# Kernel optimization log

Hardware: AMD Instinct MI355X
Metric: run time of the kernel (lower is better)

The kernel has to match this reference:

```python
import jax, jax.numpy as jnp
import numpy as np

N_QUBITS = 12
N_LAYERS = 2
PATCH = 16
NPS = 14  # patches per side for 224/16
N_PATCHES = NPS * NPS
SCALE = 1.0 / np.sqrt(N_QUBITS)


def _butterfly_gates(n):
    # Faithful replication of QuantumOrthogonalLayer.butterfly_circuit indexing:
    # param_idx increments even when the (idx1, idx2) pair is skipped.
    gates, pidx = [], 0
    n_bl = int(np.ceil(np.log2(n)))
    for layer in range(n_bl):
        stride = 2 ** layer
        for start in range(0, n - stride, 2 * stride):
            for off in range(stride):
                i1, i2 = start + off, start + off + stride
                if i1 < n and i2 < n:
                    gates.append((pidx, i1, i2))
                pidx += 1
    nppl = sum(2 ** (n_bl - 1 - i) * 2 ** i for i in range(n_bl))  # n_params() = 32
    return gates, nppl

GATES, NPPL = _butterfly_gates(N_QUBITS)

# Pauli-Z sign table: qubit 0 is the most-significant bit of the flattened state index.
_bits = (np.arange(2 ** N_QUBITS)[:, None] >> np.arange(N_QUBITS - 1, -1, -1)[None, :]) & 1
Z_SIGNS = jnp.asarray(1.0 - 2.0 * _bits, dtype=jnp.float32)  # (4096, 12)


def _rbs_u(theta):
    # 4x4 real unitary of RY(2t,w1); CNOT(w1,w2); RY(-2t,w1); CNOT(w1,w2)
    c, s = jnp.cos(theta), jnp.sin(theta)
    c2, s2, cs = c * c, s * s, c * s
    return jnp.stack([
        jnp.stack([c2, s2, -cs, cs]),
        jnp.stack([s2, c2, cs, -cs]),
        jnp.stack([cs, -cs, c2, s2]),
        jnp.stack([-cs, cs, s2, c2]),
    ])


def _apply_2q(state, U, i, j):
    # state: (P, 2, 2, ..., 2); apply U to qubit axes i, j
    st = jnp.moveaxis(state, (1 + i, 1 + j), (-2, -1))
    shp = st.shape
    st = st.reshape(shp[:-2] + (4,)) @ U.T
    return jnp.moveaxis(st.reshape(shp), (-2, -1), (1 + i, 1 + j))


@jax.checkpoint
def quantum_expvals(features, params):
    # features: (P, n_qubits) angles; params: (N_LAYERS * NPPL,)
    P = features.shape[0]
    half = 0.5 * features
    amp = jnp.stack([jnp.cos(half), jnp.sin(half)], axis=-1)  # (P, n, 2) RY(x)|0>
    state = jnp.ones((P, 1), features.dtype)
    for q in range(N_QUBITS):  # product-state angle encoding
        state = (state[:, :, None] * amp[:, q][:, None, :]).reshape(P, -1)
    state = state.reshape((P,) + (2,) * N_QUBITS)
    for l in range(N_LAYERS):
        base = l * NPPL
        for pidx, w1, w2 in GATES:
            state = _apply_2q(state, _rbs_u(params[base + pidx]), w1, w2)
    probs = state.reshape(P, -1) ** 2
    return probs @ Z_SIGNS  # (P, n_qubits) <Z_i>


def setup_inputs() -> dict:
    key = jax.random.key(0)
    ks = jax.random.split(key, 6)
    x = jax.random.normal(ks[0], (4, 3, 224, 224), dtype=jnp.float32)
    W_proj = jax.random.normal(ks[1], (N_QUBITS, PATCH * PATCH), dtype=jnp.float32) / np.sqrt(PATCH * PATCH)
    b_proj = jnp.zeros((N_QUBITS,), jnp.float32)
    q_params = 0.1 * jax.random.normal(ks[2], (N_LAYERS * NPPL,), dtype=jnp.float32)
    k_params = 0.1 * jax.random.normal(ks[3], (N_LAYERS * NPPL,), dtype=jnp.float32)
    v_params = 0.1 * jax.random.normal(ks[4], (N_LAYERS * NPPL,), dtype=jnp.float32)
    W_cls = jax.random.normal(ks[5], (1000, N_PATCHES * N_QUBITS), dtype=jnp.float32) / np.sqrt(N_PATCHES * N_QUBITS)
    b_cls = jnp.zeros((1000,), jnp.float32)
    return {"x": x, "W_proj": W_proj, "b_proj": b_proj, "q_params": q_params,
            "k_params": k_params, "v_params": v_params, "W_cls": W_cls, "b_cls": b_cls}


def reference(x, W_proj, b_proj, q_params, k_params, v_params, W_cls, b_cls):
    B = x.shape[0]
    xg = jnp.mean(x, axis=1)  # channel average -> (B, H, W)
    patches = xg.reshape(B, NPS, PATCH, NPS, PATCH).transpose(0, 1, 3, 2, 4)
    patches = patches.reshape(B, N_PATCHES, PATCH * PATCH)
    proj = patches @ W_proj.T + b_proj  # (B, n_patches, n_qubits)
    feats = proj.reshape(-1, N_QUBITS)
    Q = quantum_expvals(feats, q_params).reshape(B, N_PATCHES, N_QUBITS)
    K = quantum_expvals(feats, k_params).reshape(B, N_PATCHES, N_QUBITS)
    V = quantum_expvals(feats, v_params).reshape(B, N_PATCHES, N_QUBITS)
    attn = jax.nn.softmax(jnp.einsum('bqd,bkd->bqk', Q, K) * SCALE, axis=-1)
    out = jnp.einsum('bqk,bkd->bqd', attn, V)  # (B, n_patches, n_qubits)
    logits = out.reshape(B, -1) @ W_cls.T + b_cls
    return logits
```

## Files before the change

kernel.cpp:

```cpp
#include <hip/hip_runtime.h>
#include <math.h>

#define NQ        12
#define NPS       14
#define NPATCH    196
#define NB        4
#define NCLS      1000
#define FEATDIM   2352
#define SCALE_F   0.28867513459481287f
#define LSTRIDE   65

constexpr int PR[5][6] = {
    { 6, 7, 8, 9,10,11},
    { 2, 3, 4, 5, 6, 7},
    { 0, 1, 2, 3, 7,11},
    { 1, 2, 5, 6, 9,10},
    { 0, 4, 8, 9,10,11},
};
constexpr int PT[5][6] = {
    { 0, 1, 2, 3, 4, 5},
    { 8, 9, 0, 1,10,11},
    { 9, 4, 8, 6, 5,10},
    { 0, 8, 4, 7, 3,11},
    { 6, 5, 1, 2, 3, 7},
};

constexpr int wgt(int X, int pos) {
    for (int k = 0; k < 6; ++k) if (PR[X][k] == pos) return 1 << k;
    for (int k = 0; k < 6; ++k) if (PT[X][k] == pos) return LSTRIDE << k;
    return 0;
}
constexpr int rimm(int X, int Y, int r) {
    int s = 0;
    for (int j = 0; j < 6; ++j) if ((r >> j) & 1) s += wgt(X, PR[Y][j]);
    return s;
}

template<int X, int Y>
__device__ __forceinline__ void relayout(float amp[64], float* lds, int tid) {
    float* w = lds + LSTRIDE * tid;
    #pragma unroll
    for (int r = 0; r < 64; ++r) w[r] = amp[r];
    __syncthreads();
    int base = 0;
    #pragma unroll
    for (int j = 0; j < 6; ++j)
        base += ((tid >> j) & 1) ? wgt(X, PT[Y][j]) : 0;
    #pragma unroll
    for (int r = 0; r < 64; ++r)
        amp[r] = lds[base + rimm(X, Y, r)];
    __syncthreads();
}

template<int MI, int MJ>
__device__ __forceinline__ void apply_gate(float amp[64], float gc, float gs) {
    #pragma unroll
    for (int m = 0; m < 64; ++m) {
        if (m & (MI | MJ)) continue;
        float a0 = amp[m], a1 = amp[m | MJ], a2 = amp[m | MI], a3 = amp[m | MI | MJ];
        float p  = a0 + a1, q  = a0 - a1;
        float p2 = a2 + a3, q2 = a2 - a3;
        float t1 = 0.5f * p  + gc * q  - gs * q2;
        float t2 = 0.5f * p2 + gc * q2 + gs * q;
        amp[m]           = t1;
        amp[m | MJ]      = p  - t1;
        amp[m | MI]      = t2;
        amp[m | MI | MJ] = p2 - t2;
    }
}

__global__ __launch_bounds__(64) void qcirc_kernel(
    const float* __restrict__ x,
    const float* __restrict__ Wp,
    const float* __restrict__ bproj,
    const float* __restrict__ qp,
    const float* __restrict__ kp,
    const float* __restrict__ vp,
    float* __restrict__ qkv)
{
    __shared__ __align__(16) float lds[64 * LSTRIDE];
    __shared__ float chs[NQ], shs[NQ];
    __shared__ float gC[40], gS[40];
    __shared__ float psum[NQ];

    const int tid = threadIdx.x;
    const int p = blockIdx.x, b = blockIdx.y, c = blockIdx.z;
    const int bp = b * NPATCH + p;
    const float* params = (c == 0) ? qp : (c == 1) ? kp : vp;

    float part[NQ];
    #pragma unroll
    for (int q = 0; q < NQ; ++q) part[q] = 0.0f;
    {
        int py = p / NPS, px = p % NPS;
        const float* xb = x + (size_t)b * 3 * 224 * 224;
        #pragma unroll
        for (int k = 0; k < 4; ++k) {
            int pix = tid + 64 * k;
            int off = (py * 16 + (pix >> 4)) * 224 + px * 16 + (pix & 15);
            float v = (xb[off] + xb[off + 50176] + xb[off + 100352]) * (1.0f / 3.0f);
            #pragma unroll
            for (int q = 0; q < NQ; ++q) part[q] += v * Wp[q * 256 + pix];
        }
    }
    if (tid < 40) {
        int l = tid / 20, g = tid - l * 20;
        float th = params[l * 32 + g];
        gC[tid] = 0.5f * cosf(2.0f * th);
        gS[tid] = 0.5f * sinf(2.0f * th);
    }
    #pragma unroll
    for (int o = 1; o < 64; o <<= 1) {
        #pragma unroll
        for (int q = 0; q < NQ; ++q) part[q] += __shfl_xor(part[q], o);
    }
    if (tid == 0) {
        #pragma unroll
        for (int q = 0; q < NQ; ++q) psum[q] = part[q];
    }
    __syncthreads();
    if (tid < NQ) {
        float h = 0.5f * (psum[tid] + bproj[tid]);
        chs[tid] = cosf(h); shs[tid] = sinf(h);
    }
    __syncthreads();

    float amp[64];
    {
        float hi = 1.0f;
        #pragma unroll
        for (int j = 0; j < 6; ++j)
            hi *= ((tid >> j) & 1) ? shs[11 - j] : chs[11 - j];
        float pl[8], ph[8];
        #pragma unroll
        for (int i = 0; i < 8; ++i) {
            pl[i] = ((i & 4) ? shs[0] : chs[0]) * ((i & 2) ? shs[1] : chs[1]) *
                    ((i & 1) ? shs[2] : chs[2]) * hi;
            ph[i] = ((i & 4) ? shs[3] : chs[3]) * ((i & 2) ? shs[4] : chs[4]) *
                    ((i & 1) ? shs[5] : chs[5]);
        }
        #pragma unroll
        for (int r = 0; r < 64; ++r) amp[r] = pl[r >> 3] * ph[r & 7];
    }

    #pragma unroll 1
    for (int l = 0; l < 2; ++l) {
        const int bb = l * 20;
        apply_gate<32,16>(amp, gC[bb+0], gS[bb+0]);
        apply_gate< 8, 4>(amp, gC[bb+1], gS[bb+1]);
        apply_gate< 2, 1>(amp, gC[bb+2], gS[bb+2]);
        apply_gate<32, 8>(amp, gC[bb+6], gS[bb+6]);
        apply_gate<16, 4>(amp, gC[bb+7], gS[bb+7]);
        relayout<0,1>(amp, lds, tid);
        apply_gate< 8, 4>(amp, gC[bb+3], gS[bb+3]);
        apply_gate< 2, 1>(amp, gC[bb+4], gS[bb+4]);
        apply_gate<32, 8>(amp, gC[bb+8], gS[bb+8]);
        apply_gate<16, 4>(amp, gC[bb+9], gS[bb+9]);
        relayout<1,2>(amp, lds, tid);
        apply_gate< 2, 1>(amp, gC[bb+5],  gS[bb+5]);
        apply_gate< 8, 2>(amp, gC[bb+10], gS[bb+10]);
        apply_gate< 4, 1>(amp, gC[bb+11], gS[bb+11]);
        apply_gate<32,16>(amp, gC[bb+12], gS[bb+12]);
        apply_gate<32, 8>(amp, gC[bb+16], gS[bb+16]);
        relayout<2,3>(amp, lds, tid);
        apply_gate<32, 8>(amp, gC[bb+13], gS[bb+13]);
        apply_gate<16, 4>(amp, gC[bb+14], gS[bb+14]);
        apply_gate<32, 2>(amp, gC[bb+17], gS[bb+17]);
        apply_gate<16, 1>(amp, gC[bb+18], gS[bb+18]);
        relayout<3,4>(amp, lds, tid);
        apply_gate< 4, 2>(amp, gC[bb+15], gS[bb+15]);
        apply_gate< 4, 1>(amp, gC[bb+19], gS[bb+19]);
        if (l == 0) relayout<4,0>(amp, lds, tid);
    }

    float Sq11, Sq7, Sq3, Sq2, Sq1, Sq0, T;
    {
        float s1[32]; Sq11 = 0.0f;
        #pragma unroll
        for (int i = 0; i < 32; ++i) {
            float e = amp[2*i] * amp[2*i], o = amp[2*i+1] * amp[2*i+1];
            s1[i] = e + o; Sq11 += e - o;
        }
        float s2[16]; Sq7 = 0.0f;
        #pragma unroll
        for (int i = 0; i < 16; ++i) { s2[i] = s1[2*i] + s1[2*i+1]; Sq7 += s1[2*i] - s1[2*i+1]; }
        float s3[8]; Sq3 = 0.0f;
        #pragma unroll
        for (int i = 0; i < 8; ++i) { s3[i] = s2[2*i] + s2[2*i+1]; Sq3 += s2[2*i] - s2[2*i+1]; }
        float s4[4]; Sq2 = 0.0f;
        #pragma unroll
        for (int i = 0; i < 4; ++i) { s4[i] = s3[2*i] + s3[2*i+1]; Sq2 += s3[2*i] - s3[2*i+1]; }
        float s5[2]; Sq1 = 0.0f;
        #pragma unroll
        for (int i = 0; i < 2; ++i) { s5[i] = s4[2*i] + s4[2*i+1]; Sq1 += s4[2*i] - s4[2*i+1]; }
        T = s5[0] + s5[1]; Sq0 = s5[0] - s5[1];
    }
    float A = T, M[6];
    #pragma unroll
    for (int pbit = 0; pbit < 6; ++pbit) {
        int msk = 1 << pbit;
        float Ap = __shfl_xor(A, msk);
        float d  = A - Ap;
        M[pbit] = (tid & msk) ? -d : d;
        A += Ap;
        #pragma unroll
        for (int k = 0; k < 6; ++k)
            if (k < pbit) M[k] += __shfl_xor(M[k], msk);
        Sq0  += __shfl_xor(Sq0,  msk);
        Sq1  += __shfl_xor(Sq1,  msk);
        Sq2  += __shfl_xor(Sq2,  msk);
        Sq3  += __shfl_xor(Sq3,  msk);
        Sq7  += __shfl_xor(Sq7,  msk);
        Sq11 += __shfl_xor(Sq11, msk);
    }
    if (tid == 0) {
        float* out = qkv + ((size_t)c * (NB * NPATCH) + bp) * NQ;
        out[0]  = Sq0;  out[1]  = Sq1;  out[2]  = Sq2;  out[3]  = Sq3;
        out[4]  = M[5]; out[5]  = M[0]; out[6]  = M[1]; out[7]  = Sq7;
        out[8]  = M[4]; out[9]  = M[3]; out[10] = M[2]; out[11] = Sq11;
    }
}

__global__ __launch_bounds__(256) void attn_kernel(
    const float* __restrict__ qkv,
    float* __restrict__ outb)
{
    int tid = threadIdx.x;
    int qp = blockIdx.x, b = blockIdx.y;
    const float* Q = qkv;
    const float* K = qkv + NB * NPATCH * NQ;
    const float* V = qkv + 2 * NB * NPATCH * NQ;

    __shared__ float redm[4], reds[4], redv[4][NQ];

    float qv[NQ];
    #pragma unroll
    for (int d = 0; d < NQ; d++) qv[d] = Q[(b * NPATCH + qp) * NQ + d];

    float score = -1e30f;
    if (tid < NPATCH) {
        float s = 0.0f;
        #pragma unroll
        for (int d = 0; d < NQ; d++) s += qv[d] * K[(b * NPATCH + tid) * NQ + d];
        score = s * SCALE_F;
    }
    float m = score;
    #pragma unroll
    for (int o = 32; o > 0; o >>= 1) m = fmaxf(m, __shfl_down(m, o));
    int lane = tid & 63, wv = tid >> 6;
    if (lane == 0) redm[wv] = m;
    __syncthreads();
    float maxv = fmaxf(fmaxf(redm[0], redm[1]), fmaxf(redm[2], redm[3]));

    float w = (tid < NPATCH) ? expf(score - maxv) : 0.0f;
    float sm = w;
    #pragma unroll
    for (int o = 32; o > 0; o >>= 1) sm += __shfl_down(sm, o);
    if (lane == 0) reds[wv] = sm;

    float part[NQ];
    #pragma unroll
    for (int d = 0; d < NQ; d++) part[d] = 0.0f;
    if (tid < NPATCH) {
        #pragma unroll
        for (int d = 0; d < NQ; d++) part[d] = w * V[(b * NPATCH + tid) * NQ + d];
    }
    #pragma unroll
    for (int d = 0; d < NQ; d++) {
        #pragma unroll
        for (int o = 32; o > 0; o >>= 1) part[d] += __shfl_down(part[d], o);
    }
    if (lane == 0) {
        #pragma unroll
        for (int d = 0; d < NQ; d++) redv[wv][d] = part[d];
    }
    __syncthreads();
    if (tid < NQ) {
        float sumv = reds[0] + reds[1] + reds[2] + reds[3];
        float s = redv[0][tid] + redv[1][tid] + redv[2][tid] + redv[3][tid];
        outb[(size_t)b * FEATDIM + qp * NQ + tid] = s / sumv;
    }
}

__global__ __launch_bounds__(256) void cls_kernel(
    const float* __restrict__ outb,
    const float* __restrict__ Wc,
    const float* __restrict__ bc,
    float* __restrict__ logits)
{
    int o = blockIdx.x, tid = threadIdx.x;
    float acc[NB] = {0.0f, 0.0f, 0.0f, 0.0f};
    const float* wrow = Wc + (size_t)o * FEATDIM;
    for (int j = tid; j < FEATDIM; j += 256) {
        float w = wrow[j];
        #pragma unroll
        for (int b = 0; b < NB; b++) acc[b] += w * outb[(size_t)b * FEATDIM + j];
    }
    #pragma unroll
    for (int b = 0; b < NB; b++) {
        #pragma unroll
        for (int off = 32; off > 0; off >>= 1) acc[b] += __shfl_down(acc[b], off);
    }
    __shared__ float red[4][NB];
    int lane = tid & 63, wv = tid >> 6;
    if (lane == 0) {
        #pragma unroll
        for (int b = 0; b < NB; b++) red[wv][b] = acc[b];
    }
    __syncthreads();
    if (tid < NB) {
        float s = red[0][tid] + red[1][tid] + red[2][tid] + red[3][tid];
        logits[(size_t)tid * NCLS + o] = s + bc[o];
    }
}

extern "C" void kernel_launch(void* const* d_in, const int* in_sizes, int n_in,
                              void* d_out, int out_size, void* d_ws, size_t ws_size,
                              hipStream_t stream) {
    const float* x     = (const float*)d_in[0];
    const float* Wp    = (const float*)d_in[1];
    const float* bproj = (const float*)d_in[2];
    const float* qp    = (const float*)d_in[3];
    const float* kp    = (const float*)d_in[4];
    const float* vp    = (const float*)d_in[5];
    const float* Wc    = (const float*)d_in[6];
    const float* bc    = (const float*)d_in[7];
    float* logits = (float*)d_out;

    float* ws   = (float*)d_ws;
    float* qkv  = ws;
    float* outb = ws + 28224;

    qcirc_kernel<<<dim3(NPATCH, NB, 3), 64, 0, stream>>>(x, Wp, bproj, qp, kp, vp, qkv);
    attn_kernel <<<dim3(NPATCH, NB),   256, 0, stream>>>(qkv, outb);
    cls_kernel  <<<NCLS,               256, 0, stream>>>(outb, Wc, bc, logits);
}
```

Measured before the change: 136.9 us.

## Split quantum state over 128 threads with 32 amplitudes each, vectorize attn/cls loads

The circuit kernel now spreads the 4096-amplitude state across two wavefronts (128 threads) holding 32 amplitudes each instead of 64. The qubit-to-register/lane mappings and the LDS relayout schedule are rebuilt with six permutations, and partial sums are combined across the two waves through shared memory. This cuts per-thread register pressure and raises occupancy and parallelism, at the cost of an extra relayout per layer and cross-wave reductions. The attention and classifier kernels also switch to float4 vector loads.

```diff
diff --git a/kernel.cpp b/kernel.cpp
--- a/kernel.cpp
+++ b/kernel.cpp
@@ -8,54 +8,56 @@
 #define NCLS      1000
 #define FEATDIM   2352
 #define SCALE_F   0.28867513459481287f
-#define LSTRIDE   65
-
-constexpr int PR[5][6] = {
-    { 6, 7, 8, 9,10,11},
-    { 2, 3, 4, 5, 6, 7},
-    { 0, 1, 2, 3, 7,11},
-    { 1, 2, 5, 6, 9,10},
-    { 0, 4, 8, 9,10,11},
+#define LSTRIDE   33
+
+constexpr int PR[6][5] = {
+    {11,10, 9, 8, 7},
+    { 7, 6, 5, 4, 3},
+    { 3, 2, 1, 0,11},
+    {11,10, 7, 6, 3},
+    {10, 9, 5, 2, 1},
+    { 9, 8, 4, 1, 0},
 };
-constexpr int PT[5][6] = {
-    { 0, 1, 2, 3, 4, 5},
-    { 8, 9, 0, 1,10,11},
-    { 9, 4, 8, 6, 5,10},
-    { 0, 8, 4, 7, 3,11},
-    { 6, 5, 1, 2, 3, 7},
+constexpr int PT[6][7] = {
+    { 5, 4, 3, 1, 2, 0, 6},
+    {11,10, 2, 1, 9, 8, 0},
+    { 8, 7, 6, 9, 5, 4,10},
+    { 5, 8, 2, 1, 0, 4, 9},
+    {11, 7, 8, 4, 6, 3, 0},
+    { 5, 3,10, 7, 6, 2,11},
 };
 
 constexpr int wgt(int X, int pos) {
-    for (int k = 0; k < 6; ++k) if (PR[X][k] == pos) return 1 << k;
-    for (int k = 0; k < 6; ++k) if (PT[X][k] == pos) return LSTRIDE << k;
+    for (int k = 0; k < 5; ++k) if (PR[X][k] == pos) return 1 << k;
+    for (int k = 0; k < 7; ++k) if (PT[X][k] == pos) return LSTRIDE << k;
     return 0;
 }
 constexpr int rimm(int X, int Y, int r) {
     int s = 0;
-    for (int j = 0; j < 6; ++j) if ((r >> j) & 1) s += wgt(X, PR[Y][j]);
+    for (int j = 0; j < 5; ++j) if ((r >> j) & 1) s += wgt(X, PR[Y][j]);
     return s;
 }
 
 template<int X, int Y>
-__device__ __forceinline__ void relayout(float amp[64], float* lds, int tid) {
+__device__ __forceinline__ void relayout(float amp[32], float* lds, int tid) {
     float* w = lds + LSTRIDE * tid;
     #pragma unroll
-    for (int r = 0; r < 64; ++r) w[r] = amp[r];
+    for (int r = 0; r < 32; ++r) w[r] = amp[r];
     __syncthreads();
     int base = 0;
     #pragma unroll
-    for (int j = 0; j < 6; ++j)
+    for (int j = 0; j < 7; ++j)
         base += ((tid >> j) & 1) ? wgt(X, PT[Y][j]) : 0;
     #pragma unroll
-    for (int r = 0; r < 64; ++r)
+    for (int r = 0; r < 32; ++r)
         amp[r] = lds[base + rimm(X, Y, r)];
     __syncthreads();
 }
 
 template<int MI, int MJ>
-__device__ __forceinline__ void apply_gate(float amp[64], float gc, float gs) {
-    #pragma unroll
-    for (int m = 0; m < 64; ++m) {
+__device__ __forceinline__ void apply_gate(float amp[32], float gc, float gs) {
+    #pragma unroll
+    for (int m = 0; m < 32; ++m) {
         if (m & (MI | MJ)) continue;
         float a0 = amp[m], a1 = amp[m | MJ], a2 = amp[m | MI], a3 = amp[m | MI | MJ];
         float p  = a0 + a1, q  = a0 - a1;
@@ -69,7 +71,9 @@
     }
 }
 
-__global__ __launch_bounds__(64) void qcirc_kernel(
+__device__ const int SLOT[12] = {0,3,7,8,4,5,1,9,2,6,10,11};
+
+__global__ __launch_bounds__(128, 4) void qcirc_kernel(
     const float* __restrict__ x,
     const float* __restrict__ Wp,
     const float* __restrict__ bproj,
@@ -78,10 +82,10 @@
     const float* __restrict__ vp,
     float* __restrict__ qkv)
 {
-    __shared__ __align__(16) float lds[64 * LSTRIDE];
+    __shared__ __align__(16) float lds[128 * LSTRIDE];
     __shared__ float chs[NQ], shs[NQ];
     __shared__ float gC[40], gS[40];
-    __shared__ float psum[NQ];
+    __shared__ float red2[2][12];
 
     const int tid = threadIdx.x;
     const int p = blockIdx.x, b = blockIdx.y, c = blockIdx.z;
@@ -95,8 +99,8 @@
         int py = p / NPS, px = p % NPS;
         const float* xb = x + (size_t)b * 3 * 224 * 224;
         #pragma unroll
-        for (int k = 0; k < 4; ++k) {
-            int pix = tid + 64 * k;
+        for (int k = 0; k < 2; ++k) {
+            int pix = tid + 128 * k;
             int off = (py * 16 + (pix >> 4)) * 224 + px * 16 + (pix & 15);
             float v = (xb[off] + xb[off + 50176] + xb[off + 100352]) * (1.0f / 3.0f);
             #pragma unroll
@@ -114,86 +118,90 @@
         #pragma unroll
         for (int q = 0; q < NQ; ++q) part[q] += __shfl_xor(part[q], o);
     }
-    if (tid == 0) {
-        #pragma unroll
-        for (int q = 0; q < NQ; ++q) psum[q] = part[q];
+    {
+        int lane = tid & 63, wv = tid >> 6;
+        if (lane == 0) {
+            #pragma unroll
+            for (int q = 0; q < NQ; ++q) red2[wv][q] = part[q];
+        }
     }
     __syncthreads();
     if (tid < NQ) {
-        float h = 0.5f * (psum[tid] + bproj[tid]);
+        float h = 0.5f * (red2[0][tid] + red2[1][tid] + bproj[tid]);
         chs[tid] = cosf(h); shs[tid] = sinf(h);
     }
     __syncthreads();
 
-    float amp[64];
-    {
-        float hi = 1.0f;
-        #pragma unroll
-        for (int j = 0; j < 6; ++j)
-            hi *= ((tid >> j) & 1) ? shs[11 - j] : chs[11 - j];
-        float pl[8], ph[8];
-        #pragma unroll
-        for (int i = 0; i < 8; ++i) {
-            pl[i] = ((i & 4) ? shs[0] : chs[0]) * ((i & 2) ? shs[1] : chs[1]) *
-                    ((i & 1) ? shs[2] : chs[2]) * hi;
-            ph[i] = ((i & 4) ? shs[3] : chs[3]) * ((i & 2) ? shs[4] : chs[4]) *
-                    ((i & 1) ? shs[5] : chs[5]);
-        }
-        #pragma unroll
-        for (int r = 0; r < 64; ++r) amp[r] = pl[r >> 3] * ph[r & 7];
+    float amp[32];
+    {
+        float hi = ((tid &  1) ? shs[6]  : chs[6])  *
+                   ((tid &  2) ? shs[7]  : chs[7])  *
+                   ((tid &  4) ? shs[8]  : chs[8])  *
+                   ((tid &  8) ? shs[10] : chs[10]) *
+                   ((tid & 16) ? shs[9]  : chs[9])  *
+                   ((tid & 32) ? shs[11] : chs[11]) *
+                   ((tid & 64) ? shs[5]  : chs[5]);
+        float pA[8], pB[4];
+        #pragma unroll
+        for (int i = 0; i < 8; ++i)
+            pA[i] = ((i & 1) ? shs[0] : chs[0]) * ((i & 2) ? shs[1] : chs[1]) *
+                    ((i & 4) ? shs[2] : chs[2]);
+        #pragma unroll
+        for (int i = 0; i < 4; ++i)
+            pB[i] = ((i & 1) ? shs[3] : chs[3]) * ((i & 2) ? shs[4] : chs[4]);
+        #pragma unroll
+        for (int r = 0; r < 32; ++r) amp[r] = pA[r & 7] * pB[r >> 3] * hi;
     }
 
     #pragma unroll 1
     for (int l = 0; l < 2; ++l) {
         const int bb = l * 20;
-        apply_gate<32,16>(amp, gC[bb+0], gS[bb+0]);
-        apply_gate< 8, 4>(amp, gC[bb+1], gS[bb+1]);
-        apply_gate< 2, 1>(amp, gC[bb+2], gS[bb+2]);
-        apply_gate<32, 8>(amp, gC[bb+6], gS[bb+6]);
-        apply_gate<16, 4>(amp, gC[bb+7], gS[bb+7]);
+        apply_gate<1, 2>(amp, gC[bb+0], gS[bb+0]);
+        apply_gate<4, 8>(amp, gC[bb+1], gS[bb+1]);
+        apply_gate<1, 4>(amp, gC[bb+6], gS[bb+6]);
+        apply_gate<2, 8>(amp, gC[bb+7], gS[bb+7]);
         relayout<0,1>(amp, lds, tid);
-        apply_gate< 8, 4>(amp, gC[bb+3], gS[bb+3]);
-        apply_gate< 2, 1>(amp, gC[bb+4], gS[bb+4]);
-        apply_gate<32, 8>(amp, gC[bb+8], gS[bb+8]);
-        apply_gate<16, 4>(amp, gC[bb+9], gS[bb+9]);
+        apply_gate<1, 2>(amp, gC[bb+2], gS[bb+2]);
+        apply_gate<4, 8>(amp, gC[bb+3], gS[bb+3]);
+        apply_gate<1, 4>(amp, gC[bb+8], gS[bb+8]);
+        apply_gate<2, 8>(amp, gC[bb+9], gS[bb+9]);
         relayout<1,2>(amp, lds, tid);
-        apply_gate< 2, 1>(amp, gC[bb+5],  gS[bb+5]);
-        apply_gate< 8, 2>(amp, gC[bb+10], gS[bb+10]);
-        apply_gate< 4, 1>(amp, gC[bb+11], gS[bb+11]);
-        apply_gate<32,16>(amp, gC[bb+12], gS[bb+12]);
-        apply_gate<32, 8>(amp, gC[bb+16], gS[bb+16]);
+        apply_gate<1, 2>(amp, gC[bb+4],  gS[bb+4]);
+        apply_gate<4, 8>(amp, gC[bb+5],  gS[bb+5]);
+        apply_gate<1, 4>(amp, gC[bb+10], gS[bb+10]);
+        apply_gate<2, 8>(amp, gC[bb+11], gS[bb+11]);
         relayout<2,3>(amp, lds, tid);
-        apply_gate<32, 8>(amp, gC[bb+13], gS[bb+13]);
-        apply_gate<16, 4>(amp, gC[bb+14], gS[bb+14]);
-        apply_gate<32, 2>(amp, gC[bb+17], gS[bb+17]);
-        apply_gate<16, 1>(amp, gC[bb+18], gS[bb+18]);
+        apply_gate<1, 4>(amp, gC[bb+12], gS[bb+12]);
+        apply_gate<2, 8>(amp, gC[bb+13], gS[bb+13]);
+        apply_gate<1,16>(amp, gC[bb+16], gS[bb+16]);
         relayout<3,4>(amp, lds, tid);
-        apply_gate< 4, 2>(amp, gC[bb+15], gS[bb+15]);
-        apply_gate< 4, 1>(amp, gC[bb+19], gS[bb+19]);
-        if (l == 0) relayout<4,0>(amp, lds, tid);
-    }
-
-    float Sq11, Sq7, Sq3, Sq2, Sq1, Sq0, T;
-    {
-        float s1[32]; Sq11 = 0.0f;
-        #pragma unroll
-        for (int i = 0; i < 32; ++i) {
+        apply_gate<2, 4>(amp, gC[bb+14], gS[bb+14]);
+        apply_gate<1, 8>(amp, gC[bb+17], gS[bb+17]);
+        relayout<4,5>(amp, lds, tid);
+        apply_gate<2, 4>(amp, gC[bb+15], gS[bb+15]);
+        apply_gate<1, 8>(amp, gC[bb+18], gS[bb+18]);
+        apply_gate<2,16>(amp, gC[bb+19], gS[bb+19]);
+        if (l == 0) relayout<5,0>(amp, lds, tid);
+    }
+
+    float T, Sq2, Sq3, Sq7, Sq10, Sq11;
+    {
+        float t1[16]; Sq2 = 0.0f;
+        #pragma unroll
+        for (int i = 0; i < 16; ++i) {
             float e = amp[2*i] * amp[2*i], o = amp[2*i+1] * amp[2*i+1];
-            s1[i] = e + o; Sq11 += e - o;
-        }
-        float s2[16]; Sq7 = 0.0f;
-        #pragma unroll
-        for (int i = 0; i < 16; ++i) { s2[i] = s1[2*i] + s1[2*i+1]; Sq7 += s1[2*i] - s1[2*i+1]; }
-        float s3[8]; Sq3 = 0.0f;
-        #pragma unroll
-        for (int i = 0; i < 8; ++i) { s3[i] = s2[2*i] + s2[2*i+1]; Sq3 += s2[2*i] - s2[2*i+1]; }
-        float s4[4]; Sq2 = 0.0f;
-        #pragma unroll
-        for (int i = 0; i < 4; ++i) { s4[i] = s3[2*i] + s3[2*i+1]; Sq2 += s3[2*i] - s3[2*i+1]; }
-        float s5[2]; Sq1 = 0.0f;
-        #pragma unroll
-        for (int i = 0; i < 2; ++i) { s5[i] = s4[2*i] + s4[2*i+1]; Sq1 += s4[2*i] - s4[2*i+1]; }
-        T = s5[0] + s5[1]; Sq0 = s5[0] - s5[1];
+            t1[i] = e + o; Sq2 += e - o;
+        }
+        float t2[8]; Sq3 = 0.0f;
+        #pragma unroll
+        for (int i = 0; i < 8; ++i) { t2[i] = t1[2*i] + t1[2*i+1]; Sq3 += t1[2*i] - t1[2*i+1]; }
+        float t3[4]; Sq7 = 0.0f;
+        #pragma unroll
+        for (int i = 0; i < 4; ++i) { t3[i] = t2[2*i] + t2[2*i+1]; Sq7 += t2[2*i] - t2[2*i+1]; }
+        float t4[2]; Sq10 = 0.0f;
+        #pragma unroll
+        for (int i = 0; i < 2; ++i) { t4[i] = t3[2*i] + t3[2*i+1]; Sq10 += t3[2*i] - t3[2*i+1]; }
+        T = t4[0] + t4[1]; Sq11 = t4[0] - t4[1];
     }
     float A = T, M[6];
     #pragma unroll
@@ -206,18 +214,32 @@
         #pragma unroll
         for (int k = 0; k < 6; ++k)
             if (k < pbit) M[k] += __shfl_xor(M[k], msk);
-        Sq0  += __shfl_xor(Sq0,  msk);
-        Sq1  += __shfl_xor(Sq1,  msk);
         Sq2  += __shfl_xor(Sq2,  msk);
         Sq3  += __shfl_xor(Sq3,  msk);
         Sq7  += __shfl_xor(Sq7,  msk);
+        Sq10 += __shfl_xor(Sq10, msk);
         Sq11 += __shfl_xor(Sq11, msk);
     }
-    if (tid == 0) {
-        float* out = qkv + ((size_t)c * (NB * NPATCH) + bp) * NQ;
-        out[0]  = Sq0;  out[1]  = Sq1;  out[2]  = Sq2;  out[3]  = Sq3;
-        out[4]  = M[5]; out[5]  = M[0]; out[6]  = M[1]; out[7]  = Sq7;
-        out[8]  = M[4]; out[9]  = M[3]; out[10] = M[2]; out[11] = Sq11;
+    {
+        int lane = tid & 63, wv = tid >> 6;
+        if (lane == 0) {
+            red2[wv][0] = A;
+            red2[wv][1] = M[0];
+            red2[wv][2] = M[1];
+            red2[wv][3] = M[2];
+            red2[wv][4] = M[3];
+            red2[wv][5] = M[4];
+            red2[wv][6] = M[5];
+            red2[wv][7] = Sq2;  red2[wv][8]  = Sq3;
+            red2[wv][9] = Sq7;  red2[wv][10] = Sq10; red2[wv][11] = Sq11;
+        }
+    }
+    __syncthreads();
+    if (tid < NQ) {
+        int sl = SLOT[tid];
+        float v0 = red2[0][sl], v1 = red2[1][sl];
+        float s = (tid == 0) ? (v0 - v1) : (v0 + v1);
+        qkv[((size_t)c * (NB * NPATCH) + bp) * NQ + tid] = s;
     }
 }
 
@@ -233,16 +255,21 @@
 
     __shared__ float redm[4], reds[4], redv[4][NQ];
 
-    float qv[NQ];
-    #pragma unroll
-    for (int d = 0; d < NQ; d++) qv[d] = Q[(b * NPATCH + qp) * NQ + d];
+    float4 q0 = ((const float4*)(Q + (b * NPATCH + qp) * NQ))[0];
+    float4 q1 = ((const float4*)(Q + (b * NPATCH + qp) * NQ))[1];
+    float4 q2 = ((const float4*)(Q + (b * NPATCH + qp) * NQ))[2];
 
     float score = -1e30f;
+    float4 v0, v1, v2;
     if (tid < NPATCH) {
-        float s = 0.0f;
-        #pragma unroll
-        for (int d = 0; d < NQ; d++) s += qv[d] * K[(b * NPATCH + tid) * NQ + d];
+        const float4* K4 = (const float4*)(K + (b * NPATCH + tid) * NQ);
+        float4 k0 = K4[0], k1 = K4[1], k2 = K4[2];
+        float s = q0.x*k0.x + q0.y*k0.y + q0.z*k0.z + q0.w*k0.w
+                + q1.x*k1.x + q1.y*k1.y + q1.z*k1.z + q1.w*k1.w
+                + q2.x*k2.x + q2.y*k2.y + q2.z*k2.z + q2.w*k2.w;
         score = s * SCALE_F;
+        const float4* V4 = (const float4*)(V + (b * NPATCH + tid) * NQ);
+        v0 = V4[0]; v1 = V4[1]; v2 = V4[2];
     }
     float m = score;
     #pragma unroll
@@ -262,8 +289,9 @@
     #pragma unroll
     for (int d = 0; d < NQ; d++) part[d] = 0.0f;
     if (tid < NPATCH) {
-        #pragma unroll
-        for (int d = 0; d < NQ; d++) part[d] = w * V[(b * NPATCH + tid) * NQ + d];
+        part[0] = w*v0.x; part[1] = w*v0.y; part[2]  = w*v0.z; part[3]  = w*v0.w;
+        part[4] = w*v1.x; part[5] = w*v1.y; part[6]  = w*v1.z; part[7]  = w*v1.w;
+        part[8] = w*v2.x; part[9] = w*v2.y; part[10] = w*v2.z; part[11] = w*v2.w;
     }
     #pragma unroll
     for (int d = 0; d < NQ; d++) {
@@ -290,11 +318,14 @@
 {
     int o = blockIdx.x, tid = threadIdx.x;
     float acc[NB] = {0.0f, 0.0f, 0.0f, 0.0f};
-    const float* wrow = Wc + (size_t)o * FEATDIM;
-    for (int j = tid; j < FEATDIM; j += 256) {
-        float w = wrow[j];
-        #pragma unroll
-        for (int b = 0; b < NB; b++) acc[b] += w * outb[(size_t)b * FEATDIM + j];
+    const float4* w4 = (const float4*)(Wc + (size_t)o * FEATDIM);
+    for (int j = tid; j < FEATDIM / 4; j += 256) {
+        float4 w = w4[j];
+        #pragma unroll
+        for (int b = 0; b < NB; b++) {
+            float4 ov = ((const float4*)(outb + (size_t)b * FEATDIM))[j];
+            acc[b] += w.x*ov.x + w.y*ov.y + w.z*ov.z + w.w*ov.w;
+        }
     }
     #pragma unroll
     for (int b = 0; b < NB; b++) {
@@ -331,7 +362,7 @@
     float* qkv  = ws;
     float* outb = ws + 28224;
 
-    qcirc_kernel<<<dim3(NPATCH, NB, 3), 64, 0, stream>>>(x, Wp, bproj, qp, kp, vp, qkv);
-    attn_kernel <<<dim3(NPATCH, NB),   256, 0, stream>>>(qkv, outb);
-    cls_kernel  <<<NCLS,               256, 0, stream>>>(outb, Wc, bc, logits);
-}
+    qcirc_kernel<<<dim3(NPATCH, NB, 3), 128, 0, stream>>>(x, Wp, bproj, qp, kp, vp, qkv);
+    attn_kernel <<<dim3(NPATCH, NB),    256, 0, stream>>>(qkv, outb);
+    cls_kernel  <<<NCLS,                256, 0, stream>>>(outb, Wc, bc, logits);
+}
```

Measured after the change: 125.6 us. 8.2% less time.
